# Optimization experiments

Hardware: AMD Instinct MI355X
Metric: run time of the kernel (lower is better)

The kernel has to match this reference:

```python
import jax, jax.numpy as jnp
import numpy as np

TEXT_VOCAB = 32000
NUM_CODEBOOKS = 8
CODEBOOK_SIZE = 1024
SLICE = CODEBOOK_SIZE + 2  # codebook slice length incl. BOS/EOS
AUDIO_VOCAB = NUM_CODEBOOKS * SLICE  # 8208
HIDDEN = 2048
NH = 16
NKV = 8
HD = HIDDEN // NH  # 128
FFN = 8192
LAYERS = 2
EPS = 1e-5


def setup_inputs() -> dict:
    key = jax.random.key(0)
    ks = jax.random.split(key, 16)
    s = 0.02
    qkv_dim = (NH + 2 * NKV) * HD  # 4096
    inp = {
        "input_ids": jax.random.randint(ks[0], (2, 1024), 0, TEXT_VOCAB + CODEBOOK_SIZE, dtype=jnp.int32),
        "vocab_embed": jax.random.normal(ks[1], (TEXT_VOCAB, HIDDEN), jnp.float32) * s,
        "audio_embed": jax.random.normal(ks[2], (AUDIO_VOCAB, HIDDEN), jnp.float32) * s,
        "ln_in": jnp.ones((LAYERS, HIDDEN), jnp.float32),
        "ln_audio_in": jnp.ones((LAYERS, HIDDEN), jnp.float32),
        "ln_post": jnp.ones((LAYERS, HIDDEN), jnp.float32),
        "ln_audio_post": jnp.ones((LAYERS, HIDDEN), jnp.float32),
        "w_qkv": jax.random.normal(ks[3], (LAYERS, HIDDEN, qkv_dim), jnp.float32) * s,
        "w_o": jax.random.normal(ks[4], (LAYERS, NH * HD, HIDDEN), jnp.float32) * s,
        "w_fc": jax.random.normal(ks[5], (LAYERS, HIDDEN, FFN), jnp.float32) * s,
        "w_proj": jax.random.normal(ks[6], (LAYERS, FFN, HIDDEN), jnp.float32) * s,
        "w_audio_fc": jax.random.normal(ks[7], (LAYERS, HIDDEN, FFN), jnp.float32) * s,
        "w_audio_proj": jax.random.normal(ks[8], (LAYERS, FFN, HIDDEN), jnp.float32) * s,
        "ln_f": jnp.ones((HIDDEN,), jnp.float32),
    }
    return inp


def _rms(x, w):
    return x * jax.lax.rsqrt(jnp.mean(x * x, axis=-1, keepdims=True) + EPS) * w


def reference(input_ids, vocab_embed, audio_embed, ln_in, ln_audio_in, ln_post,
              ln_audio_post, w_qkv, w_o, w_fc, w_proj, w_audio_fc, w_audio_proj, ln_f):
    B, S = input_ids.shape
    audio_mask = input_ids > TEXT_VOCAB - 1  # [B,S] bool
    mask3 = audio_mask[..., None]

    # --- embedding ---
    text_ids = jnp.where(audio_mask, TEXT_VOCAB - 1, input_ids)
    text_e = vocab_embed[text_ids]  # [B,S,H]
    audio_ids = jnp.where(audio_mask, input_ids - TEXT_VOCAB, 0)
    shift = jnp.arange(NUM_CODEBOOKS, dtype=jnp.int32) * SLICE  # [C]
    audio_e = audio_embed[audio_ids[None] + shift[:, None, None]].sum(0)  # [B,S,H]
    h = jnp.where(mask3, audio_e, text_e)

    causal = jnp.tril(jnp.ones((S, S), bool))
    scale = 1.0 / np.sqrt(HD)

    def layer(h, p):
        li, lai, lp, lap, wqkv, wo, wfc, wpr, wafc, wapr = p
        # dual-path input norm (both computed, merged by mask)
        x = jnp.where(mask3, _rms(h, lai), _rms(h, li))
        # causal GQA attention
        qkv = x @ wqkv
        q = qkv[..., : NH * HD].reshape(B, S, NH, HD)
        k = qkv[..., NH * HD:(NH + NKV) * HD].reshape(B, S, NKV, HD)
        v = qkv[..., (NH + NKV) * HD:].reshape(B, S, NKV, HD)
        rep = NH // NKV
        k = jnp.repeat(k, rep, axis=2)
        v = jnp.repeat(v, rep, axis=2)
        scores = jnp.einsum('bqhd,bkhd->bhqk', q, k) * scale
        scores = jnp.where(causal, scores, jnp.finfo(scores.dtype).min)
        attn = jax.nn.softmax(scores, axis=-1)
        o = jnp.einsum('bhqk,bkhd->bqhd', attn, v).reshape(B, S, NH * HD) @ wo
        h = h + o
        # dual-path FFN (both computed, merged by mask)
        y_text = jax.nn.silu(_rms(h, lp) @ wfc) @ wpr
        y_audio = jax.nn.silu(_rms(h, lap) @ wafc) @ wapr
        h = h + jnp.where(mask3, y_audio, y_text)
        return h, None

    params = (ln_in, ln_audio_in, ln_post, ln_audio_post,
              w_qkv, w_o, w_fc, w_proj, w_audio_fc, w_audio_proj)
    h, _ = jax.lax.scan(layer, h, params)
    return _rms(h, ln_f)
```

## Files before the change

### kernel.cpp

```cpp
#include <hip/hip_runtime.h>
#include <hip/hip_bf16.h>

typedef unsigned short u16;
typedef __attribute__((ext_vector_type(4))) float f32x4;
typedef __attribute__((ext_vector_type(8))) short bf16x8;
typedef __attribute__((ext_vector_type(8))) unsigned short u16x8;
typedef __attribute__((ext_vector_type(4))) unsigned short u16x4;

#define BM 128
#define BN 128
#define BK 64

__device__ __forceinline__ u16 f2bf(float f) {
  union { float f; unsigned u; } v; v.f = f;
  unsigned r = v.u + 0x7FFFu + ((v.u >> 16) & 1u);
  return (u16)(r >> 16);
}
__device__ __forceinline__ float bf2f(u16 v) {
  union { float f; unsigned u; } x; x.u = (unsigned)v << 16; return x.f;
}

__device__ __forceinline__ int xswz(int wg, int n) {
  return (wg & 7) * (n >> 3) + (wg >> 3);
}

__device__ __forceinline__ void g8_stage_half(
    const u16* __restrict__ G, int ldg, int tile, int half, u16* ldsbase) {
  const int tid = threadIdx.x;
#pragma unroll
  for (int load = 0; load < 2; ++load) {
    int unit = load * 512 + tid;
    int row = unit >> 3;
    int seg = (unit & 7) ^ ((unit >> 3) & 7);
    __builtin_amdgcn_global_load_lds(
        (const __attribute__((address_space(1))) void*)(G + (size_t)(half * 128 + row) * ldg + tile * 64 + seg * 8),
        (__attribute__((address_space(3))) void*)(ldsbase + half * 8192 + load * 4096 + (tid >> 6) * 512),
        16, 0, 0);
  }
}

__device__ __forceinline__ void g8_core(
    const u16* __restrict__ A, int lda, const u16* __restrict__ Bt, int ldb,
    int NT, u16* lds, f32x4 acc[8][4]) {
  const int tid = threadIdx.x;
  const int lane = tid & 63;
  const int wid = tid >> 6;
  const int wr = wid >> 2, wc = wid & 3;
  const int lr = lane & 15;
  const int lk4 = lane >> 4;
  const int sw = lane & 7;
  const int off0 = ((lk4 ^ sw) * 8);
  const int off1 = (((4 + lk4) ^ sw) * 8);

  u16* ldsA = lds;
  u16* ldsB = lds + 32768;

  g8_stage_half(A, lda, 0, 0, ldsA);
  g8_stage_half(A, lda, 0, 1, ldsA);
  g8_stage_half(Bt, ldb, 0, 0, ldsB);
  g8_stage_half(Bt, ldb, 0, 1, ldsB);
  if (NT > 1) {
    g8_stage_half(Bt, ldb, 1, 0, ldsB + 16384);
    g8_stage_half(Bt, ldb, 1, 1, ldsB + 16384);
  }
  asm volatile("s_waitcnt vmcnt(4)" ::: "memory");
  __builtin_amdgcn_s_barrier();
  __builtin_amdgcn_sched_barrier(0);

  for (int g = 0; g < NT; ++g) {
    const int buf = g & 1;
    const u16* cA = ldsA + buf * 16384 + wr * 8192;
    const u16* cB = ldsB + buf * 16384;
    bf16x8 bv[4][2];
#pragma unroll
    for (int p = 0; p < 4; ++p) {
      bf16x8 av[2][2];
      if (p == 0) {
#pragma unroll
        for (int n = 0; n < 4; ++n) {
          int rg = wc * 64 + n * 16 + lr;
          const u16* rbase = &cB[(rg >> 7) * 8192 + (rg & 127) * 64];
          bv[n][0] = *(const bf16x8*)&rbase[off0];
          bv[n][1] = *(const bf16x8*)&rbase[off1];
        }
      }
#pragma unroll
      for (int m2 = 0; m2 < 2; ++m2) {
        const u16* rbase = &cA[((p * 2 + m2) * 16 + lr) * 64];
        av[m2][0] = *(const bf16x8*)&rbase[off0];
        av[m2][1] = *(const bf16x8*)&rbase[off1];
      }

      if (p == 0 && g + 1 < NT) g8_stage_half(A, lda, g + 1, 0, ldsA + ((g + 1) & 1) * 16384);
      if (p == 1 && g + 1 < NT) g8_stage_half(A, lda, g + 1, 1, ldsA + ((g + 1) & 1) * 16384);
      if (p == 2 && g + 2 < NT) g8_stage_half(Bt, ldb, g + 2, 0, ldsB + buf * 16384);
      if (p == 3) {
        if (g + 2 < NT) {
          g8_stage_half(Bt, ldb, g + 2, 1, ldsB + buf * 16384);
          asm volatile("s_waitcnt vmcnt(4)" ::: "memory");
        } else if (g + 1 < NT) {
          asm volatile("s_waitcnt vmcnt(0)" ::: "memory");
        }
      }
      __builtin_amdgcn_s_barrier();
      asm volatile("s_waitcnt lgkmcnt(0)" ::: "memory");
      __builtin_amdgcn_sched_barrier(0);
      __builtin_amdgcn_s_setprio(1);
#pragma unroll
      for (int m2 = 0; m2 < 2; ++m2)
#pragma unroll
        for (int n = 0; n < 4; ++n)
#pragma unroll
          for (int kk = 0; kk < 2; ++kk)
            acc[p * 2 + m2][n] = __builtin_amdgcn_mfma_f32_16x16x32_bf16(
                av[m2][kk], bv[n][kk], acc[p * 2 + m2][n], 0, 0, 0);
      __builtin_amdgcn_s_setprio(0);
      __builtin_amdgcn_sched_barrier(0);
      __builtin_amdgcn_s_barrier();
    }
  }
}

__device__ __forceinline__ void g8_acc_zero(f32x4 acc[8][4]) {
#pragma unroll
  for (int m = 0; m < 8; ++m)
#pragma unroll
    for (int n = 0; n < 4; ++n)
      acc[m][n] = (f32x4){0.f, 0.f, 0.f, 0.f};
}

__global__ __launch_bounds__(512, 2) void k_gemm8_qkv(
    const u16* __restrict__ A, const u16* __restrict__ Bt, u16* __restrict__ Pq) {
  __shared__ u16 lds[65536];
  const int wg = xswz(blockIdx.x, 256);
  const int ks = wg >> 7, rem = wg & 127;
  const int tm = rem >> 4, tn = rem & 15;
  f32x4 acc[8][4];
  g8_acc_zero(acc);
  g8_core(A + (size_t)tm * 256 * 2048 + ks * 1024, 2048,
          Bt + (size_t)tn * 256 * 2048 + ks * 1024, 2048, 16, lds, acc);
  const int lane = threadIdx.x & 63, wid = threadIdx.x >> 6;
  const int wr = wid >> 2, wc = wid & 3;
  const int col = lane & 15, rb = (lane >> 4) * 4;
#pragma unroll
  for (int m = 0; m < 8; ++m)
#pragma unroll
    for (int n = 0; n < 4; ++n)
#pragma unroll
      for (int j = 0; j < 4; ++j) {
        int gm = tm * 256 + wr * 128 + m * 16 + rb + j;
        int gn = tn * 256 + wc * 64 + n * 16 + col;
        Pq[((size_t)ks * 2048 + gm) * 4096 + gn] = f2bf(acc[m][n][j]);
      }
}

__global__ __launch_bounds__(512, 2) void k_gemm8_fc(
    const u16* __restrict__ A, const u16* __restrict__ Bt, u16* __restrict__ Cb) {
  __shared__ u16 lds[65536];
  const int wg = xswz(blockIdx.x, 256);
  const int tm = wg >> 5, tn = wg & 31;
  f32x4 acc[8][4];
  g8_acc_zero(acc);
  g8_core(A + (size_t)tm * 256 * 2048, 2048, Bt + (size_t)tn * 256 * 2048, 2048, 32, lds, acc);
  const int lane = threadIdx.x & 63, wid = threadIdx.x >> 6;
  const int wr = wid >> 2, wc = wid & 3;
  const int col = lane & 15, rb = (lane >> 4) * 4;
#pragma unroll
  for (int m = 0; m < 8; ++m)
#pragma unroll
    for (int n = 0; n < 4; ++n)
#pragma unroll
      for (int j = 0; j < 4; ++j) {
        int gm = tm * 256 + wr * 128 + m * 16 + rb + j;
        int gn = tn * 256 + wc * 64 + n * 16 + col;
        float v = acc[m][n][j];
        Cb[(size_t)gm * 8192 + gn] = f2bf(v / (1.f + __expf(-v)));
      }
}

__global__ __launch_bounds__(512, 2) void k_gemm8_sk(
    const u16* __restrict__ A, int lda, const u16* __restrict__ Bt, int ldb,
    int NT, int koff, u16* __restrict__ Pp) {
  __shared__ u16 lds[65536];
  const int wg = xswz(blockIdx.x, 256);
  const int ks = wg >> 6, rem = wg & 63;
  const int tm = rem >> 3, tn = rem & 7;
  f32x4 acc[8][4];
  g8_acc_zero(acc);
  g8_core(A + (size_t)tm * 256 * lda + ks * koff, lda,
          Bt + (size_t)tn * 256 * ldb + ks * koff, ldb, NT, lds, acc);
  const int lane = threadIdx.x & 63, wid = threadIdx.x >> 6;
  const int wr = wid >> 2, wc = wid & 3;
  const int col = lane & 15, rb = (lane >> 4) * 4;
#pragma unroll
  for (int m = 0; m < 8; ++m)
#pragma unroll
    for (int n = 0; n < 4; ++n)
#pragma unroll
      for (int j = 0; j < 4; ++j) {
        int gm = tm * 256 + wr * 128 + m * 16 + rb + j;
        int gn = tn * 256 + wc * 64 + n * 16 + col;
        Pp[((size_t)ks * 2048 + gm) * 2048 + gn] = f2bf(acc[m][n][j]);
      }
}

__global__ __launch_bounds__(256) void k_red_qkv(
    const u16* __restrict__ Pq, u16* __restrict__ Q, u16* __restrict__ Kb,
    u16* __restrict__ VT) {
  const int gm = blockIdx.y;
  const int c = blockIdx.x * 1024 + threadIdx.x * 4;
  const size_t i = (size_t)gm * 4096 + c;
  u16x4 a = *(const u16x4*)&Pq[i];
  u16x4 b2 = *(const u16x4*)&Pq[(size_t)2048 * 4096 + i];
  const int b = gm >> 10, s = gm & 1023;
  u16 v[4];
#pragma unroll
  for (int j = 0; j < 4; ++j) v[j] = f2bf(bf2f(a[j]) + bf2f(b2[j]));
  const int d = c & 127;
  if (c < 2048) {
    int hh = c >> 7;
    *(u16x4*)&Q[((size_t)((b * 16 + hh) * 1024 + s)) * 128 + d] = *(u16x4*)v;
  } else if (c < 3072) {
    int kv = (c - 2048) >> 7;
    *(u16x4*)&Kb[((size_t)((b * 8 + kv) * 1024 + s)) * 128 + d] = *(u16x4*)v;
  } else {
    int kv = (c - 3072) >> 7;
#pragma unroll
    for (int j = 0; j < 4; ++j)
      VT[((size_t)((b * 8 + kv) * 128 + d + j)) * 1024 + s] = v[j];
  }
}

__device__ __forceinline__ void fa_stage128(const u16* __restrict__ G, int ldg, u16* dst,
                                            int nloads) {
  const int tid = threadIdx.x;
  for (int ld = 0; ld < nloads; ++ld) {
    int unit = ld * 256 + tid;
    int row = unit >> 4;
    int seg = (unit & 15) ^ (row & 7);
    __builtin_amdgcn_global_load_lds(
        (const __attribute__((address_space(1))) void*)(G + (size_t)row * ldg + seg * 8),
        (__attribute__((address_space(3))) void*)(dst + ld * 2048 + (tid >> 6) * 512),
        16, 0, 0);
  }
}
__device__ __forceinline__ void fa_stage64(const u16* __restrict__ G, int ldg, u16* dst,
                                           int nloads) {
  const int tid = threadIdx.x;
  for (int ld = 0; ld < nloads; ++ld) {
    int unit = ld * 256 + tid;
    int row = unit >> 3;
    int seg = (unit & 7) ^ (row & 7);
    __builtin_amdgcn_global_load_lds(
        (const __attribute__((address_space(1))) void*)(G + (size_t)row * ldg + seg * 8),
        (__attribute__((address_space(3))) void*)(dst + ld * 2048 + (tid >> 6) * 512),
        16, 0, 0);
  }
}

__global__ __launch_bounds__(256, 2) void k_fattn(
    const u16* __restrict__ Q, const u16* __restrict__ Kb, const u16* __restrict__ VT,
    u16* __restrict__ O) {
  const int tm = blockIdx.x;
  const int bh = blockIdx.y;
  const int b = bh >> 4, hq = bh & 15, kv = hq >> 1;
  __shared__ u16 lds[32768];
  u16* Klds = lds;
  u16* Vlds = lds + 8192;
  u16* Plds = lds + 24576;
  const int lane = threadIdx.x & 63, wave = threadIdx.x >> 6;
  const int wm = wave * 32;
  const int lr = lane & 15, lk = lane >> 4;
  const int rb = lk * 4;
  const int cl = lr;

  const u16* Qg = Q + ((size_t)(b * 16 + hq) * 1024 + tm * 128) * 128;
  fa_stage128(Qg, 128, lds, 8);
  asm volatile("s_waitcnt vmcnt(0)" ::: "memory");
  __builtin_amdgcn_s_barrier();
  __builtin_amdgcn_sched_barrier(0);
  bf16x8 qf[2][4];
#pragma unroll
  for (int m = 0; m < 2; ++m)
#pragma unroll
    for (int kk = 0; kk < 4; ++kk) {
      int row = wm + m * 16 + lr;
      qf[m][kk] = *(const bf16x8*)&lds[row * 128 + (((kk * 4 + lk) ^ (lr & 7)) * 8)];
    }
  asm volatile("s_waitcnt lgkmcnt(0)" ::: "memory");
  __builtin_amdgcn_s_barrier();
  __builtin_amdgcn_sched_barrier(0);

  const u16* Kg = Kb + (size_t)(b * 8 + kv) * 1024 * 128;
  const u16* Vg = VT + (size_t)(b * 8 + kv) * 128 * 1024;
  const int NT = 2 * (tm + 1);
  fa_stage128(Kg, 128, Klds, 4);
  fa_stage64(Vg, 1024, Vlds, 4);

  f32x4 accO[2][8];
#pragma unroll
  for (int m = 0; m < 2; ++m)
#pragma unroll
    for (int n = 0; n < 8; ++n) accO[m][n] = (f32x4){0.f, 0.f, 0.f, 0.f};
  float mst[8], lst[8];
#pragma unroll
  for (int i = 0; i < 8; ++i) { mst[i] = -3.0e38f; lst[i] = 0.f; }
  const float scale = 0.08838834764831845f;

  for (int t = 0; t < NT; ++t) {
    asm volatile("s_waitcnt vmcnt(0)" ::: "memory");
    __builtin_amdgcn_s_barrier();
    __builtin_amdgcn_sched_barrier(0);
    u16* Vcur = Vlds + (t & 1) * 8192;
    f32x4 accS[2][4];
#pragma unroll
    for (int m = 0; m < 2; ++m)
#pragma unroll
      for (int n = 0; n < 4; ++n) accS[m][n] = (f32x4){0.f, 0.f, 0.f, 0.f};
#pragma unroll
    for (int kk = 0; kk < 4; ++kk) {
      bf16x8 kf[4];
#pragma unroll
      for (int n = 0; n < 4; ++n)
        kf[n] = *(const bf16x8*)&Klds[(n * 16 + lr) * 128 + (((kk * 4 + lk) ^ (lr & 7)) * 8)];
#pragma unroll
      for (int m = 0; m < 2; ++m)
#pragma unroll
        for (int n = 0; n < 4; ++n)
          accS[m][n] = __builtin_amdgcn_mfma_f32_16x16x32_bf16(qf[m][kk], kf[n], accS[m][n], 0, 0, 0);
    }
    asm volatile("s_waitcnt lgkmcnt(0)" ::: "memory");
    __builtin_amdgcn_s_barrier();
    __builtin_amdgcn_sched_barrier(0);
    if (t + 1 < NT) {
      fa_stage128(Kg + (size_t)(t + 1) * 64 * 128, 128, Klds, 4);
      fa_stage64(Vg + (t + 1) * 64, 1024, Vlds + ((t + 1) & 1) * 8192, 4);
    }
    const bool dm = (t >= 2 * tm);
#pragma unroll
    for (int m = 0; m < 2; ++m)
#pragma unroll
      for (int j = 0; j < 4; ++j) {
        const int si = m * 4 + j;
        const int rglob = tm * 128 + wm + m * 16 + rb + j;
        float v[4];
        float vmax = -3.0e38f;
#pragma unroll
        for (int n = 0; n < 4; ++n) {
          float x = accS[m][n][j] * scale;
          if (dm && (t * 64 + n * 16 + cl > rglob)) x = -3.0e38f;
          v[n] = x;
          vmax = fmaxf(vmax, x);
        }
#pragma unroll
        for (int o = 1; o < 16; o <<= 1) vmax = fmaxf(vmax, __shfl_xor(vmax, o));
        float mnew = fmaxf(mst[si], vmax);
        float alpha = __expf(mst[si] - mnew);
        mst[si] = mnew;
        float rs = 0.f;
        const int prow = wm + m * 16 + rb + j;
#pragma unroll
        for (int n = 0; n < 4; ++n) {
          float pp = __expf(v[n] - mnew);
          rs += pp;
          int col = n * 16 + cl;
          Plds[prow * 64 + (((col >> 3) ^ (prow & 7)) * 8) + (col & 7)] = f2bf(pp);
        }
#pragma unroll
        for (int o = 1; o < 16; o <<= 1) rs += __shfl_xor(rs, o);
        lst[si] = lst[si] * alpha + rs;
#pragma unroll
        for (int n = 0; n < 8; ++n) accO[m][n][j] *= alpha;
      }
#pragma unroll
    for (int kk = 0; kk < 2; ++kk) {
      bf16x8 pf[2], vf[8];
#pragma unroll
      for (int m = 0; m < 2; ++m) {
        int prow = wm + m * 16 + lr;
        pf[m] = *(const bf16x8*)&Plds[prow * 64 + (((kk * 4 + lk) ^ (lr & 7)) * 8)];
      }
#pragma unroll
      for (int n = 0; n < 8; ++n) {
        int d = n * 16 + lr;
        vf[n] = *(const bf16x8*)&Vcur[d * 64 + (((kk * 4 + lk) ^ (d & 7)) * 8)];
      }
#pragma unroll
      for (int m = 0; m < 2; ++m)
#pragma unroll
        for (int n = 0; n < 8; ++n)
          accO[m][n] = __builtin_amdgcn_mfma_f32_16x16x32_bf16(pf[m], vf[n], accO[m][n], 0, 0, 0);
    }
  }
#pragma unroll
  for (int m = 0; m < 2; ++m)
#pragma unroll
    for (int j = 0; j < 4; ++j) {
      float invl = 1.f / lst[m * 4 + j];
      int s = tm * 128 + wm + m * 16 + rb + j;
#pragma unroll
      for (int n = 0; n < 8; ++n) {
        int d = n * 16 + cl;
        O[(size_t)(b * 1024 + s) * 2048 + hq * 128 + d] = f2bf(accO[m][n][j] * invl);
      }
    }
}

__device__ __forceinline__ void acc_zero(f32x4 acc[4][4]) {
#pragma unroll
  for (int m = 0; m < 4; ++m)
#pragma unroll
    for (int n = 0; n < 4; ++n)
      acc[m][n] = (f32x4){0.f, 0.f, 0.f, 0.f};
}

__global__ __launch_bounds__(256) void k_gemm_csf(
    const u16* __restrict__ A, int lda, const float* __restrict__ Wf, int ldw,
    int ksteps, int ntn, u16* __restrict__ Pp, const int* __restrict__ cnt) {
  const int Na = cnt[0];
  const int tm = blockIdx.y;
  if (tm * 128 >= Na) return;
  const int tn = blockIdx.x % ntn;
  const int ks = blockIdx.x / ntn;
  const int ldc = ntn * 128;
  const int k0 = ks * ksteps * BK;
  __shared__ u16 sA[2 * BM * BK], sB[2 * BN * BK];
  f32x4 acc[4][4];
  acc_zero(acc);

  const u16* Ab = A + (size_t)tm * 128 * lda + k0;
  const float* Wb = Wf + (size_t)k0 * ldw + tn * 128;

  const int tid = threadIdx.x;
  const int wave = tid >> 6, lane = tid & 63;
  const int r = tid >> 3;
  const int ksw = (tid & 7) ^ ((tid >> 3) & 7);
  const int wm = (wave >> 1) * 64, wn = (wave & 1) * 64;
  const int lr = lane & 15, lk4 = lane >> 4, sw = lane & 7;
  const int off0 = ((lk4 ^ sw) * 8), off1 = (((4 + lk4) ^ sw) * 8);
  const int amax = Na - 1 - tm * 128;
  const int bk_ = tid >> 5;
  const int bn4 = (tid & 31) * 4;

  f32x4 breg[8];

  auto stageA = [&](int buf, int kt) {
    u16* dA = sA + buf * 8192 + wave * 512;
    const int kk0 = kt * BK;
#pragma unroll
    for (int i = 0; i < 4; ++i) {
      int ra = i * 32 + r; if (ra > amax) ra = amax;
      __builtin_amdgcn_global_load_lds(
          (const __attribute__((address_space(1))) void*)(Ab + (size_t)ra * lda + kk0 + ksw * 8),
          (__attribute__((address_space(3))) void*)(dA + i * 2048), 16, 0, 0);
    }
  };
  auto loadB = [&](int kt) {
#pragma unroll
    for (int i = 0; i < 8; ++i) {
      int kk_ = kt * 64 + i * 8 + bk_;
      breg[i] = __builtin_nontemporal_load((const f32x4*)&Wb[(size_t)kk_ * ldw + bn4]);
    }
  };
  auto writeB = [&](int buf) {
    u16* dB = sB + buf * 8192;
#pragma unroll
    for (int i = 0; i < 8; ++i) {
      int kk_ = i * 8 + bk_;
#pragma unroll
      for (int j = 0; j < 4; ++j) {
        int n = bn4 + j;
        dB[n * 64 + (((kk_ >> 3) ^ (n & 7)) * 8) + (kk_ & 7)] = f2bf(breg[i][j]);
      }
    }
  };

  stageA(0, 0);
  loadB(0);
  asm volatile("s_waitcnt vmcnt(0)" ::: "memory");
  writeB(0);
  asm volatile("s_waitcnt lgkmcnt(0)" ::: "memory");
  __builtin_amdgcn_s_barrier();
  __builtin_amdgcn_sched_barrier(0);

  for (int kt = 0; kt < ksteps; ++kt) {
    const int cur = kt & 1;
    if (kt + 1 < ksteps) { stageA(cur ^ 1, kt + 1); loadB(kt + 1); }
    const u16* cA = sA + cur * 8192;
    const u16* cB = sB + cur * 8192;
#pragma unroll
    for (int kk = 0; kk < 2; ++kk) {
      const int off = kk ? off1 : off0;
      bf16x8 av[4], bv[4];
#pragma unroll
      for (int m = 0; m < 4; ++m)
        av[m] = *(const bf16x8*)&cA[(wm + m * 16 + lr) * BK + off];
#pragma unroll
      for (int n = 0; n < 4; ++n)
        bv[n] = *(const bf16x8*)&cB[(wn + n * 16 + lr) * BK + off];
#pragma unroll
      for (int m = 0; m < 4; ++m)
#pragma unroll
        for (int n = 0; n < 4; ++n)
          acc[m][n] = __builtin_amdgcn_mfma_f32_16x16x32_bf16(av[m], bv[n], acc[m][n], 0, 0, 0);
    }
    asm volatile("s_waitcnt vmcnt(0)" ::: "memory");
    if (kt + 1 < ksteps) writeB(cur ^ 1);
    asm volatile("s_waitcnt lgkmcnt(0)" ::: "memory");
    __builtin_amdgcn_s_barrier();
    __builtin_amdgcn_sched_barrier(0);
  }

  const int col = lane & 15, rb = (lane >> 4) * 4;
#pragma unroll
  for (int m = 0; m < 4; ++m)
#pragma unroll
    for (int n = 0; n < 4; ++n)
#pragma unroll
      for (int j = 0; j < 4; ++j) {
        int gm = tm * 128 + wm + m * 16 + rb + j;
        int gn = tn * 128 + wn + n * 16 + col;
        Pp[((size_t)ks * 256 + gm) * ldc + gn] = f2bf(acc[m][n][j]);
      }
}

__global__ __launch_bounds__(256) void k_red8_silu(
    const u16* __restrict__ Pp, u16* __restrict__ t1, const int* __restrict__ cnt) {
  const int row = blockIdx.y;
  if (row >= cnt[0]) return;
  const int c = blockIdx.x * 1024 + threadIdx.x * 4;
  const size_t i = (size_t)row * 8192 + c;
  float s[4] = {0.f, 0.f, 0.f, 0.f};
#pragma unroll
  for (int k = 0; k < 8; ++k) {
    u16x4 a = *(const u16x4*)&Pp[(size_t)k * 256 * 8192 + i];
#pragma unroll
    for (int j = 0; j < 4; ++j) s[j] += bf2f(a[j]);
  }
  u16x4 ov;
#pragma unroll
  for (int j = 0; j < 4; ++j) {
    float v = s[j];
    ov[j] = f2bf(v / (1.f + __expf(-v)));
  }
  *(u16x4*)&t1[i] = ov;
}

__global__ __launch_bounds__(256) void k_transpose_all(
    const float* __restrict__ w_qkv, const float* __restrict__ w_o,
    const float* __restrict__ w_fc, const float* __restrict__ w_proj,
    u16* __restrict__ WtAll) {
  int bid = blockIdx.x;
  int l = 0;
  if (bid >= 11264) { l = 1; bid -= 11264; }
  const float* src;
  u16* dst;
  int K, N, t;
  u16* WtL = WtAll + (size_t)l * 46137344;
  if (bid < 2048)       { src = w_qkv  + (size_t)l * 8388608;  dst = WtL;            K = 2048; N = 4096; t = bid; }
  else if (bid < 3072)  { src = w_o    + (size_t)l * 4194304;  dst = WtL + 8388608;  K = 2048; N = 2048; t = bid - 2048; }
  else if (bid < 7168)  { src = w_fc   + (size_t)l * 16777216; dst = WtL + 12582912; K = 2048; N = 8192; t = bid - 3072; }
  else                  { src = w_proj + (size_t)l * 16777216; dst = WtL + 29360128; K = 8192; N = 2048; t = bid - 7168; }
  const int nk = K >> 6;
  const int sb = t >> 6, w = t & 63;
  const int nsbk = nk >> 3;
  const int tk = ((sb % nsbk) << 3) + (w & 7);
  const int tn = ((sb / nsbk) << 3) + (w >> 3);
  const int tid = threadIdx.x;
  __shared__ float tile[64][65];
#pragma unroll
  for (int i = 0; i < 4; ++i) {
    int idx = i * 256 + tid;
    int r = idx >> 4, c4 = (idx & 15) * 4;
    f32x4 v = __builtin_nontemporal_load(
        (const f32x4*)&src[(size_t)(tk * 64 + r) * N + tn * 64 + c4]);
    tile[r][c4]     = v[0];
    tile[r][c4 + 1] = v[1];
    tile[r][c4 + 2] = v[2];
    tile[r][c4 + 3] = v[3];
  }
  __syncthreads();
#pragma unroll
  for (int i = 0; i < 2; ++i) {
    int u = i * 256 + tid;
    int n = u >> 3, seg = u & 7;
    u16x8 ov;
#pragma unroll
    for (int j = 0; j < 8; ++j) ov[j] = f2bf(tile[seg * 8 + j][n]);
    __builtin_nontemporal_store(ov, (u16x8*)&dst[(size_t)(tn * 64 + n) * K + tk * 64 + seg * 8]);
  }
}

__global__ __launch_bounds__(256) void k_scan(
    const int* __restrict__ mask, int* __restrict__ cpos,
    int* __restrict__ cidx, int* __restrict__ cnt) {
  const int tid = threadIdx.x;
  const int lane = tid & 63, wid = tid >> 6;
  int m[8];
  int s = 0;
#pragma unroll
  for (int j = 0; j < 8; ++j) { m[j] = mask[tid * 8 + j]; s += m[j]; }
  int ps = s;
#pragma unroll
  for (int o = 1; o < 64; o <<= 1) {
    int t = __shfl_up(ps, o);
    if (lane >= o) ps += t;
  }
  __shared__ int wsum[4];
  if (lane == 63) wsum[wid] = ps;
  __syncthreads();
  int base = 0;
  for (int w = 0; w < wid; ++w) base += wsum[w];
  int run = base + ps - s;
#pragma unroll
  for (int j = 0; j < 8; ++j) {
    int row = tid * 8 + j;
    cpos[row] = run;
    if (m[j]) cidx[run] = row;
    run += m[j];
  }
  if (tid == 255) cnt[0] = run;
}

__device__ __forceinline__ float block_sum256(float v, float* red) {
  const int tid = threadIdx.x;
#pragma unroll
  for (int o = 32; o; o >>= 1) v += __shfl_xor(v, o);
  if ((tid & 63) == 0) red[tid >> 6] = v;
  __syncthreads();
  float r = red[0] + red[1] + red[2] + red[3];
  __syncthreads();
  return r;
}

__global__ __launch_bounds__(256) void k_embed_rms(
    const int* __restrict__ ids, const float* __restrict__ vocab,
    const float* __restrict__ audio, const float* __restrict__ wt,
    const float* __restrict__ wa, float* __restrict__ h, int* __restrict__ mask,
    u16* __restrict__ x) {
  const int t = blockIdx.x;
  const int tid = threadIdx.x;
  const int id = ids[t];
  const int am = (id > 31999) ? 1 : 0;
  if (tid == 0) mask[t] = am;
  float* hr = h + (size_t)t * 2048;
  const int c0 = tid * 8;
  float4 v0, v1;
  if (!am) {
    const float4* src = (const float4*)(vocab + (size_t)id * 2048);
    v0 = src[tid * 2];
    v1 = src[tid * 2 + 1];
  } else {
    const int aid = id - 32000;
    v0 = (float4){0.f, 0.f, 0.f, 0.f};
    v1 = (float4){0.f, 0.f, 0.f, 0.f};
#pragma unroll
    for (int c = 0; c < 8; ++c) {
      const float4* ap = (const float4*)(audio + (size_t)(aid + c * 1026) * 2048);
      float4 a0 = ap[tid * 2], a1 = ap[tid * 2 + 1];
      v0.x += a0.x; v0.y += a0.y; v0.z += a0.z; v0.w += a0.w;
      v1.x += a1.x; v1.y += a1.y; v1.z += a1.z; v1.w += a1.w;
    }
  }
  ((float4*)hr)[tid * 2] = v0;
  ((float4*)hr)[tid * 2 + 1] = v1;
  const float* f0 = (const float*)&v0;
  const float* f1 = (const float*)&v1;
  float ss = 0.f;
#pragma unroll
  for (int j = 0; j < 4; ++j) ss += f0[j] * f0[j] + f1[j] * f1[j];
  __shared__ float red[4];
  ss = block_sum256(ss, red);
  const float inv = rsqrtf(ss * (1.0f / 2048.0f) + 1e-5f);
  const float* w = am ? wa : wt;
  u16x8 a;
#pragma unroll
  for (int j = 0; j < 8; ++j) {
    float hv = (j < 4 ? f0[j] : f1[j - 4]) * inv;
    a[j] = f2bf(hv * w[c0 + j]);
  }
  *(u16x8*)&x[(size_t)t * 2048 + c0] = a;
}

__global__ __launch_bounds__(256) void k_redrms_post(
    float* __restrict__ h, const u16* __restrict__ Pp,
    const float* __restrict__ wt, const float* __restrict__ wa,
    const int* __restrict__ mask, u16* __restrict__ x, u16* __restrict__ xc,
    const int* __restrict__ cpos) {
  const int row = blockIdx.x, tid = threadIdx.x;
  const int c0 = tid * 8;
  const size_t base = (size_t)row * 2048 + c0;
  float4 a0 = *(const float4*)&h[base];
  float4 a1 = *(const float4*)&h[base + 4];
  float* fa0 = (float*)&a0;
  float* fa1 = (float*)&a1;
#pragma unroll
  for (int k = 0; k < 4; ++k) {
    u16x8 pv = *(const u16x8*)&Pp[(size_t)k * 2048 * 2048 + base];
#pragma unroll
    for (int j = 0; j < 4; ++j) fa0[j] += bf2f(pv[j]);
#pragma unroll
    for (int j = 0; j < 4; ++j) fa1[j] += bf2f(pv[4 + j]);
  }
  *(float4*)&h[base] = a0;
  *(float4*)&h[base + 4] = a1;
  float ss = 0.f;
#pragma unroll
  for (int j = 0; j < 4; ++j) ss += fa0[j] * fa0[j] + fa1[j] * fa1[j];
  __shared__ float red[4];
  ss = block_sum256(ss, red);
  const float inv = rsqrtf(ss * (1.0f / 2048.0f) + 1e-5f);
  u16x8 xv;
#pragma unroll
  for (int j = 0; j < 8; ++j) {
    float hv = (j < 4 ? fa0[j] : fa1[j - 4]) * inv;
    xv[j] = f2bf(hv * wt[c0 + j]);
  }
  *(u16x8*)&x[base] = xv;
  if (mask[row]) {
    u16x8 av;
#pragma unroll
    for (int j = 0; j < 8; ++j) {
      float hv = (j < 4 ? fa0[j] : fa1[j - 4]) * inv;
      av[j] = f2bf(hv * wa[c0 + j]);
    }
    *(u16x8*)&xc[(size_t)cpos[row] * 2048 + c0] = av;
  }
}

__global__ __launch_bounds__(256) void k_redrms_ffn(
    float* __restrict__ h, const u16* __restrict__ Psk, const u16* __restrict__ Pap,
    const float* __restrict__ wt, const float* __restrict__ wa,
    const float* __restrict__ wf, const int* __restrict__ mask,
    const int* __restrict__ cpos, u16* __restrict__ x, float* __restrict__ outf, int fin) {
  const int row = blockIdx.x, tid = threadIdx.x;
  const int c0 = tid * 8;
  const size_t base = (size_t)row * 2048 + c0;
  float4 a0 = *(const float4*)&h[base];
  float4 a1 = *(const float4*)&h[base + 4];
  float* fa0 = (float*)&a0;
  float* fa1 = (float*)&a1;
  if (mask[row] == 0) {
#pragma unroll
    for (int k = 0; k < 4; ++k) {
      u16x8 pv = *(const u16x8*)&Psk[(size_t)k * 2048 * 2048 + base];
#pragma unroll
      for (int j = 0; j < 4; ++j) fa0[j] += bf2f(pv[j]);
#pragma unroll
      for (int j = 0; j < 4; ++j) fa1[j] += bf2f(pv[4 + j]);
    }
  } else {
    const size_t cb = (size_t)cpos[row] * 2048 + c0;
#pragma unroll
    for (int k = 0; k < 16; ++k) {
      u16x8 pv = *(const u16x8*)&Pap[(size_t)k * 256 * 2048 + cb];
#pragma unroll
      for (int j = 0; j < 4; ++j) fa0[j] += bf2f(pv[j]);
#pragma unroll
      for (int j = 0; j < 4; ++j) fa1[j] += bf2f(pv[4 + j]);
    }
  }
  if (!fin) {
    *(float4*)&h[base] = a0;
    *(float4*)&h[base + 4] = a1;
  }
  float ss = 0.f;
#pragma unroll
  for (int j = 0; j < 4; ++j) ss += fa0[j] * fa0[j] + fa1[j] * fa1[j];
  __shared__ float red[4];
  ss = block_sum256(ss, red);
  const float inv = rsqrtf(ss * (1.0f / 2048.0f) + 1e-5f);
  if (fin) {
    float4 o0, o1;
    float* p0 = (float*)&o0;
    float* p1 = (float*)&o1;
#pragma unroll
    for (int j = 0; j < 4; ++j) {
      p0[j] = fa0[j] * inv * wf[c0 + j];
      p1[j] = fa1[j] * inv * wf[c0 + 4 + j];
    }
    *(float4*)&outf[base] = o0;
    *(float4*)&outf[base + 4] = o1;
  } else {
    const float* w = mask[row] ? wa : wt;
    u16x8 xv;
#pragma unroll
    for (int j = 0; j < 8; ++j) {
      float hv = (j < 4 ? fa0[j] : fa1[j - 4]) * inv;
      xv[j] = f2bf(hv * w[c0 + j]);
    }
    *(u16x8*)&x[base] = xv;
  }
}

extern "C" void kernel_launch(void* const* d_in, const int* in_sizes, int n_in,
                              void* d_out, int out_size, void* d_ws, size_t ws_size,
                              hipStream_t stream) {
  const int* ids = (const int*)d_in[0];
  const float* vocab = (const float*)d_in[1];
  const float* audio = (const float*)d_in[2];
  const float* ln_in = (const float*)d_in[3];
  const float* ln_audio_in = (const float*)d_in[4];
  const float* ln_post = (const float*)d_in[5];
  const float* ln_audio_post = (const float*)d_in[6];
  const float* w_qkv = (const float*)d_in[7];
  const float* w_o = (const float*)d_in[8];
  const float* w_fc = (const float*)d_in[9];
  const float* w_proj = (const float*)d_in[10];
  const float* w_afc = (const float*)d_in[11];
  const float* w_aproj = (const float*)d_in[12];
  const float* ln_f = (const float*)d_in[13];
  float* out = (float*)d_out;

  char* p = (char*)d_ws;
  auto alloc = [&](size_t bytes) {
    char* r = p;
    p += (bytes + 255) & ~(size_t)255;
    return r;
  };
  float* h   = (float*)alloc((size_t)2048 * 2048 * 4);
  u16* x     = (u16*)alloc((size_t)2048 * 2048 * 2);
  u16* xc    = (u16*)alloc((size_t)2048 * 2048 * 2);
  u16* o     = (u16*)alloc((size_t)2048 * 2048 * 2);
  int* mask  = (int*)alloc((size_t)2048 * 4);
  int* cpos  = (int*)alloc((size_t)2048 * 4);
  int* cidx  = (int*)alloc((size_t)2048 * 4);
  int* cnt   = (int*)alloc((size_t)64 * 4);
  u16* WtAll = (u16*)alloc((size_t)2 * 46137344 * 2);
  u16* Q     = (u16*)alloc((size_t)2 * 16 * 1024 * 128 * 2);
  u16* Kb    = (u16*)alloc((size_t)2 * 8 * 1024 * 128 * 2);
  u16* VT    = (u16*)alloc((size_t)2 * 8 * 1024 * 128 * 2);
  char* A    = alloc((size_t)128 * 1024 * 1024);
  char* Bg   = alloc((size_t)24 * 1024 * 1024);
  u16* t1    = (u16*)alloc((size_t)2048 * 8192 * 2);
  u16* Pq    = (u16*)A;
  u16* Psk   = (u16*)A;
  u16* Pafc  = (u16*)(A + (size_t)67108864);
  u16* Paprj = (u16*)Bg;
  (void)ws_size; (void)in_sizes; (void)n_in; (void)out_size;

  k_transpose_all<<<22528, 256, 0, stream>>>(w_qkv, w_o, w_fc, w_proj, WtAll);
  k_embed_rms<<<2048, 256, 0, stream>>>(ids, vocab, audio, ln_in, ln_audio_in, h, mask, x);
  k_scan<<<1, 256, 0, stream>>>(mask, cpos, cidx, cnt);

  for (int l = 0; l < 2; ++l) {
    u16* WtL = WtAll + (size_t)l * 46137344;
    u16* Wqkv_t  = WtL;
    u16* Wo_t    = WtL + 8388608;
    u16* Wfc_t   = WtL + 12582912;
    u16* Wproj_t = WtL + 29360128;

    k_gemm8_qkv<<<256, 512, 0, stream>>>(x, Wqkv_t, Pq);
    k_red_qkv<<<dim3(4, 2048), 256, 0, stream>>>(Pq, Q, Kb, VT);
    k_fattn<<<dim3(8, 32), 256, 0, stream>>>(Q, Kb, VT, o);
    k_gemm8_sk<<<256, 512, 0, stream>>>(o, 2048, Wo_t, 2048, 8, 512, Psk);
    k_redrms_post<<<2048, 256, 0, stream>>>(h, Psk, ln_post + l * 2048,
                                            ln_audio_post + l * 2048, mask, x, xc, cpos);
    k_gemm8_fc<<<256, 512, 0, stream>>>(x, Wfc_t, t1);
    k_gemm8_sk<<<256, 512, 0, stream>>>(t1, 8192, Wproj_t, 8192, 32, 2048, Psk);
    k_gemm_csf<<<dim3(64 * 8, 2), 256, 0, stream>>>(
        xc, 2048, w_afc + (size_t)l * 2048 * 8192, 8192, 4, 64, Pafc, cnt);
    k_red8_silu<<<dim3(8, 256), 256, 0, stream>>>(Pafc, t1, cnt);
    k_gemm_csf<<<dim3(16 * 16, 2), 256, 0, stream>>>(
        t1, 8192, w_aproj + (size_t)l * 8192 * 2048, 2048, 8, 16, Paprj, cnt);
    if (l == 0)
      k_redrms_ffn<<<2048, 256, 0, stream>>>(h, Psk, Paprj, ln_in + 2048,
                                             ln_audio_in + 2048, nullptr, mask, cpos, x,
                                             nullptr, 0);
    else
      k_redrms_ffn<<<2048, 256, 0, stream>>>(h, Psk, Paprj, nullptr, nullptr, ln_f, mask,
                                             cpos, nullptr, out, 1);
  }
}
```

Baseline: 903.6 us.

## Read fp32 FFN weights directly in GEMM, dropping their pre-transpose pass

Adds a GEMM core that loads the fp32 w_fc and w_proj weights straight from global memory into registers. It converts them to bf16 and writes them into swizzled LDS in a software-pipelined way. The pre-kernel no longer transposes and casts these two large weights, which removes a full read-write pass over about 128 MB of fp32 weights per call. In exchange the FFN GEMMs read fp32 (twice the bytes) and do the conversion and LDS packing inside the main loop, which may add register pressure and LDS-write cost.

```diff
diff --git a/kernel.cpp b/kernel.cpp
--- a/kernel.cpp
+++ b/kernel.cpp
@@ -127,6 +127,121 @@
 #pragma unroll
     for (int n = 0; n < 4; ++n)
       acc[m][n] = (f32x4){0.f, 0.f, 0.f, 0.f};
+}
+
+__device__ __forceinline__ void g8f_core(
+    const u16* __restrict__ A, int lda, const float* __restrict__ W, int ldw,
+    int NT, u16* lds, f32x4 acc[8][4]) {
+  const int tid = threadIdx.x;
+  const int lane = tid & 63;
+  const int wid = tid >> 6;
+  const int wr = wid >> 2, wc = wid & 3;
+  const int lr = lane & 15;
+  const int lk4 = lane >> 4;
+  const int sw = lane & 7;
+  const int off0 = ((lk4 ^ sw) * 8);
+  const int off1 = (((4 + lk4) ^ sw) * 8);
+
+  u16* ldsA = lds;
+  u16* ldsB = lds + 32768;
+
+  const int kp = (tid & 7) * 2;
+  const int nb = (tid >> 3) * 4;
+  f32x4 breg[8];
+
+  auto loadB = [&](int g) {
+    const float* Wb = W + (size_t)(g * 64) * ldw + nb;
+#pragma unroll
+    for (int i = 0; i < 4; ++i) {
+      int k = kp + 16 * i;
+      breg[i * 2]     = *(const f32x4*)&Wb[(size_t)k * ldw];
+      breg[i * 2 + 1] = *(const f32x4*)&Wb[(size_t)(k + 1) * ldw];
+    }
+  };
+  auto writeB = [&](int g) {
+    u16* dB = ldsB + (g & 1) * 16384;
+#pragma unroll
+    for (int i = 0; i < 4; ++i) {
+      int k = kp + 16 * i;
+      int slotbase = (k >> 3);
+#pragma unroll
+      for (int j = 0; j < 4; ++j) {
+        int n = nb + j;
+        u16* base = dB + (n >> 7) * 8192 + (n & 127) * 64;
+        int slot = slotbase ^ (n & 7);
+        unsigned pack = (unsigned)f2bf(breg[i * 2][j]) |
+                        ((unsigned)f2bf(breg[i * 2 + 1][j]) << 16);
+        *(unsigned*)&base[slot * 8 + (k & 7)] = pack;
+      }
+    }
+  };
+
+  loadB(0);
+  g8_stage_half(A, lda, 0, 0, ldsA);
+  g8_stage_half(A, lda, 0, 1, ldsA);
+  asm volatile("s_waitcnt vmcnt(4)" ::: "memory");
+  writeB(0);
+  loadB(1);
+  asm volatile("s_waitcnt vmcnt(8)" ::: "memory");
+  asm volatile("s_waitcnt lgkmcnt(0)" ::: "memory");
+  __builtin_amdgcn_s_barrier();
+  __builtin_amdgcn_sched_barrier(0);
+
+  for (int g = 0; g < NT; ++g) {
+    const int buf = g & 1;
+    const u16* cA = ldsA + buf * 16384 + wr * 8192;
+    const u16* cB = ldsB + buf * 16384;
+    bf16x8 bv[4][2];
+#pragma unroll
+    for (int p = 0; p < 4; ++p) {
+      bf16x8 av[2][2];
+      if (p == 0) {
+#pragma unroll
+        for (int n = 0; n < 4; ++n) {
+          int rg = wc * 64 + n * 16 + lr;
+          const u16* rbase = &cB[(rg >> 7) * 8192 + (rg & 127) * 64];
+          bv[n][0] = *(const bf16x8*)&rbase[off0];
+          bv[n][1] = *(const bf16x8*)&rbase[off1];
+        }
+      }
+#pragma unroll
+      for (int m2 = 0; m2 < 2; ++m2) {
+        const u16* rbase = &cA[((p * 2 + m2) * 16 + lr) * 64];
+        av[m2][0] = *(const bf16x8*)&rbase[off0];
+        av[m2][1] = *(const bf16x8*)&rbase[off1];
+      }
+
+      if (p == 0 && g + 1 < NT) g8_stage_half(A, lda, g + 1, 0, ldsA + ((g + 1) & 1) * 16384);
+      if (p == 1 && g + 1 < NT) {
+        asm volatile("s_waitcnt vmcnt(2)" ::: "memory");
+        writeB(g + 1);
+        g8_stage_half(A, lda, g + 1, 1, ldsA + ((g + 1) & 1) * 16384);
+        if (g + 2 < NT) loadB(g + 2);
+      }
+      if (p == 3) {
+        if (g + 2 < NT) {
+          asm volatile("s_waitcnt vmcnt(8)" ::: "memory");
+        } else if (g + 1 < NT) {
+          asm volatile("s_waitcnt vmcnt(0)" ::: "memory");
+        }
+      }
+      __builtin_amdgcn_s_barrier();
+      asm volatile("s_waitcnt lgkmcnt(0)" ::: "memory");
+      __builtin_amdgcn_sched_barrier(0);
+      __builtin_amdgcn_s_setprio(1);
+#pragma unroll
+      for (int m2 = 0; m2 < 2; ++m2)
+#pragma unroll
+        for (int n = 0; n < 4; ++n)
+#pragma unroll
+          for (int kk = 0; kk < 2; ++kk)
+            acc[p * 2 + m2][n] = __builtin_amdgcn_mfma_f32_16x16x32_bf16(
+                av[m2][kk], bv[n][kk], acc[p * 2 + m2][n], 0, 0, 0);
+      __builtin_amdgcn_s_setprio(0);
+      __builtin_amdgcn_sched_barrier(0);
+      __builtin_amdgcn_s_barrier();
+    }
+  }
 }
 
 __global__ __launch_bounds__(512, 2) void k_gemm8_qkv(
@@ -154,30 +269,6 @@
       }
 }
 
-__global__ __launch_bounds__(512, 2) void k_gemm8_fc(
-    const u16* __restrict__ A, const u16* __restrict__ Bt, u16* __restrict__ Cb) {
-  __shared__ u16 lds[65536];
-  const int wg = xswz(blockIdx.x, 256);
-  const int tm = wg >> 5, tn = wg & 31;
-  f32x4 acc[8][4];
-  g8_acc_zero(acc);
-  g8_core(A + (size_t)tm * 256 * 2048, 2048, Bt + (size_t)tn * 256 * 2048, 2048, 32, lds, acc);
-  const int lane = threadIdx.x & 63, wid = threadIdx.x >> 6;
-  const int wr = wid >> 2, wc = wid & 3;
-  const int col = lane & 15, rb = (lane >> 4) * 4;
-#pragma unroll
-  for (int m = 0; m < 8; ++m)
-#pragma unroll
-    for (int n = 0; n < 4; ++n)
-#pragma unroll
-      for (int j = 0; j < 4; ++j) {
-        int gm = tm * 256 + wr * 128 + m * 16 + rb + j;
-        int gn = tn * 256 + wc * 64 + n * 16 + col;
-        float v = acc[m][n][j];
-        Cb[(size_t)gm * 8192 + gn] = f2bf(v / (1.f + __expf(-v)));
-      }
-}
-
 __global__ __launch_bounds__(512, 2) void k_gemm8_sk(
     const u16* __restrict__ A, int lda, const u16* __restrict__ Bt, int ldb,
     int NT, int koff, u16* __restrict__ Pp) {
@@ -189,6 +280,56 @@
   g8_acc_zero(acc);
   g8_core(A + (size_t)tm * 256 * lda + ks * koff, lda,
           Bt + (size_t)tn * 256 * ldb + ks * koff, ldb, NT, lds, acc);
+  const int lane = threadIdx.x & 63, wid = threadIdx.x >> 6;
+  const int wr = wid >> 2, wc = wid & 3;
+  const int col = lane & 15, rb = (lane >> 4) * 4;
+#pragma unroll
+  for (int m = 0; m < 8; ++m)
+#pragma unroll
+    for (int n = 0; n < 4; ++n)
+#pragma unroll
+      for (int j = 0; j < 4; ++j) {
+        int gm = tm * 256 + wr * 128 + m * 16 + rb + j;
+        int gn = tn * 256 + wc * 64 + n * 16 + col;
+        Pp[((size_t)ks * 2048 + gm) * 2048 + gn] = f2bf(acc[m][n][j]);
+      }
+}
+
+__global__ __launch_bounds__(512, 2) void k_gemm8f_fc(
+    const u16* __restrict__ A, const float* __restrict__ Wf, u16* __restrict__ Cb) {
+  __shared__ u16 lds[65536];
+  const int wg = xswz(blockIdx.x, 256);
+  const int tm = wg >> 5, tn = wg & 31;
+  f32x4 acc[8][4];
+  g8_acc_zero(acc);
+  g8f_core(A + (size_t)tm * 256 * 2048, 2048, Wf + tn * 256, 8192, 32, lds, acc);
+  const int lane = threadIdx.x & 63, wid = threadIdx.x >> 6;
+  const int wr = wid >> 2, wc = wid & 3;
+  const int col = lane & 15, rb = (lane >> 4) * 4;
+#pragma unroll
+  for (int m = 0; m < 8; ++m)
+#pragma unroll
+    for (int n = 0; n < 4; ++n)
+#pragma unroll
+      for (int j = 0; j < 4; ++j) {
+        int gm = tm * 256 + wr * 128 + m * 16 + rb + j;
+        int gn = tn * 256 + wc * 64 + n * 16 + col;
+        float v = acc[m][n][j];
+        Cb[(size_t)gm * 8192 + gn] = f2bf(v / (1.f + __expf(-v)));
+      }
+}
+
+__global__ __launch_bounds__(512, 2) void k_gemm8f_sk(
+    const u16* __restrict__ A, int lda, const float* __restrict__ Wf, int ldw,
+    int NT, u16* __restrict__ Pp) {
+  __shared__ u16 lds[65536];
+  const int wg = xswz(blockIdx.x, 256);
+  const int ks = wg >> 6, rem = wg & 63;
+  const int tm = rem >> 3, tn = rem & 7;
+  f32x4 acc[8][4];
+  g8_acc_zero(acc);
+  g8f_core(A + (size_t)tm * 256 * lda + ks * (NT * 64), lda,
+           Wf + (size_t)(ks * (NT * 64)) * ldw + tn * 256, ldw, NT, lds, acc);
   const int lane = threadIdx.x & 63, wid = threadIdx.x >> 6;
   const int wr = wid >> 2, wc = wid & 3;
   const int col = lane & 15, rb = (lane >> 4) * 4;
@@ -548,19 +689,16 @@
 
 __global__ __launch_bounds__(256) void k_transpose_all(
     const float* __restrict__ w_qkv, const float* __restrict__ w_o,
-    const float* __restrict__ w_fc, const float* __restrict__ w_proj,
     u16* __restrict__ WtAll) {
   int bid = blockIdx.x;
   int l = 0;
-  if (bid >= 11264) { l = 1; bid -= 11264; }
+  if (bid >= 3072) { l = 1; bid -= 3072; }
   const float* src;
   u16* dst;
   int K, N, t;
-  u16* WtL = WtAll + (size_t)l * 46137344;
-  if (bid < 2048)       { src = w_qkv  + (size_t)l * 8388608;  dst = WtL;            K = 2048; N = 4096; t = bid; }
-  else if (bid < 3072)  { src = w_o    + (size_t)l * 4194304;  dst = WtL + 8388608;  K = 2048; N = 2048; t = bid - 2048; }
-  else if (bid < 7168)  { src = w_fc   + (size_t)l * 16777216; dst = WtL + 12582912; K = 2048; N = 8192; t = bid - 3072; }
-  else                  { src = w_proj + (size_t)l * 16777216; dst = WtL + 29360128; K = 8192; N = 2048; t = bid - 7168; }
+  u16* WtL = WtAll + (size_t)l * 12582912;
+  if (bid < 2048) { src = w_qkv + (size_t)l * 8388608; dst = WtL;           K = 2048; N = 4096; t = bid; }
+  else            { src = w_o   + (size_t)l * 4194304; dst = WtL + 8388608; K = 2048; N = 2048; t = bid - 2048; }
   const int nk = K >> 6;
   const int sb = t >> 6, w = t & 63;
   const int nsbk = nk >> 3;
@@ -826,7 +964,7 @@
   int* cpos  = (int*)alloc((size_t)2048 * 4);
   int* cidx  = (int*)alloc((size_t)2048 * 4);
   int* cnt   = (int*)alloc((size_t)64 * 4);
-  u16* WtAll = (u16*)alloc((size_t)2 * 46137344 * 2);
+  u16* WtAll = (u16*)alloc((size_t)2 * 12582912 * 2);
   u16* Q     = (u16*)alloc((size_t)2 * 16 * 1024 * 128 * 2);
   u16* Kb    = (u16*)alloc((size_t)2 * 8 * 1024 * 128 * 2);
   u16* VT    = (u16*)alloc((size_t)2 * 8 * 1024 * 128 * 2);
@@ -839,16 +977,14 @@
   u16* Paprj = (u16*)Bg;
   (void)ws_size; (void)in_sizes; (void)n_in; (void)out_size;
 
-  k_transpose_all<<<22528, 256, 0, stream>>>(w_qkv, w_o, w_fc, w_proj, WtAll);
+  k_transpose_all<<<6144, 256, 0, stream>>>(w_qkv, w_o, WtAll);
   k_embed_rms<<<2048, 256, 0, stream>>>(ids, vocab, audio, ln_in, ln_audio_in, h, mask, x);
   k_scan<<<1, 256, 0, stream>>>(mask, cpos, cidx, cnt);
 
   for (int l = 0; l < 2; ++l) {
-    u16* WtL = WtAll + (size_t)l * 46137344;
-    u16* Wqkv_t  = WtL;
-    u16* Wo_t    = WtL + 8388608;
-    u16* Wfc_t   = WtL + 12582912;
-    u16* Wproj_t = WtL + 29360128;
+    u16* WtL = WtAll + (size_t)l * 12582912;
+    u16* Wqkv_t = WtL;
+    u16* Wo_t   = WtL + 8388608;
 
     k_gemm8_qkv<<<256, 512, 0, stream>>>(x, Wqkv_t, Pq);
     k_red_qkv<<<dim3(4, 2048), 256, 0, stream>>>(Pq, Q, Kb, VT);
@@ -856,8 +992,9 @@
     k_gemm8_sk<<<256, 512, 0, stream>>>(o, 2048, Wo_t, 2048, 8, 512, Psk);
     k_redrms_post<<<2048, 256, 0, stream>>>(h, Psk, ln_post + l * 2048,
                                             ln_audio_post + l * 2048, mask, x, xc, cpos);
-    k_gemm8_fc<<<256, 512, 0, stream>>>(x, Wfc_t, t1);
-    k_gemm8_sk<<<256, 512, 0, stream>>>(t1, 8192, Wproj_t, 8192, 32, 2048, Psk);
+    k_gemm8f_fc<<<256, 512, 0, stream>>>(x, w_fc + (size_t)l * 2048 * 8192, t1);
+    k_gemm8f_sk<<<256, 512, 0, stream>>>(t1, 8192, w_proj + (size_t)l * 8192 * 2048, 2048,
+                                         32, Psk);
     k_gemm_csf<<<dim3(64 * 8, 2), 256, 0, stream>>>(
         xc, 2048, w_afc + (size_t)l * 2048 * 8192, 8192, 4, 64, Pafc, cnt);
     k_red8_silu<<<dim3(8, 256), 256, 0, stream>>>(Pafc, t1, cnt);
```

Result: slower. 1.414 ms (+56.5%).
